# Optimization experiments

Measured on AMD Instinct MI355X. Metric: run time of the kernel, lower is better.

The kernel has to match this reference:

```python
import jax, jax.numpy as jnp
import numpy as np

EMBED_DIM = 768
NUM_HEADS = 12
HEAD_DIM = EMBED_DIM // NUM_HEADS
SCALE = HEAD_DIM ** -0.5


def setup_inputs() -> dict:
    key = jax.random.key(0)
    ks = jax.random.split(key, 9)
    B, S, D = 2, 2048, EMBED_DIM
    init = 1.0 / np.sqrt(D)  # ~ nn.Linear default uniform scale
    x = jax.random.normal(ks[0], (B, S, D), dtype=jnp.float32)
    Wq = jax.random.uniform(ks[1], (D, D), jnp.float32, -init, init)
    bq = jax.random.uniform(ks[2], (D,), jnp.float32, -init, init)
    Wk = jax.random.uniform(ks[3], (D, D), jnp.float32, -init, init)
    bk = jax.random.uniform(ks[4], (D,), jnp.float32, -init, init)
    Wv = jax.random.uniform(ks[5], (D, D), jnp.float32, -init, init)
    bv = jax.random.uniform(ks[6], (D,), jnp.float32, -init, init)
    Wo = jax.random.uniform(ks[7], (D, D), jnp.float32, -init, init)
    bo = jax.random.uniform(ks[8], (D,), jnp.float32, -init, init)
    return {"x": x, "Wq": Wq, "bq": bq, "Wk": Wk, "bk": bk,
            "Wv": Wv, "bv": bv, "Wo": Wo, "bo": bo}


def reference(x, Wq, bq, Wk, bk, Wv, bv, Wo, bo):
    B, S, D = x.shape
    H, Dh = NUM_HEADS, HEAD_DIM
    # projections; weights stored as (in, out) so x @ W == torch Linear with W.T
    q = (x @ Wq + bq).reshape(B, S, H, Dh).transpose(0, 2, 1, 3)  # [B,H,S,Dh]
    k = (x @ Wk + bk).reshape(B, S, H, Dh).transpose(0, 2, 1, 3)
    v = (x @ Wv + bv).reshape(B, S, H, Dh).transpose(0, 2, 1, 3)
    scores = jnp.einsum("bhqd,bhkd->bhqk", q, k) * SCALE        # [B,H,S,S]
    weights = jax.nn.softmax(scores, axis=-1)
    out = jnp.einsum("bhqk,bhkd->bhqd", weights, v)              # [B,H,S,Dh]
    out = out.transpose(0, 2, 1, 3).reshape(B, S, D)
    return out @ Wo + bo
```

## Files before the change

### kernel.cpp

```cpp
#include <hip/hip_runtime.h>
#include <math.h>

#define BB 2
#define SS 2048
#define DDIM 768
#define HH 12
#define DH 64
#define NROWS (BB*SS)
#define NQT2 (SS/128)
#define NSPLIT 4

typedef _Float16 f16;
typedef _Float16 half2v __attribute__((ext_vector_type(2)));
typedef __fp16 fp16x2 __attribute__((ext_vector_type(2)));
typedef _Float16 half4 __attribute__((ext_vector_type(4)));
typedef _Float16 half8 __attribute__((ext_vector_type(8)));
typedef float f32x4 __attribute__((ext_vector_type(4)));
typedef float f32x16 __attribute__((ext_vector_type(16)));
typedef unsigned int u32;
typedef unsigned int u32x4v __attribute__((ext_vector_type(4)));

__device__ __forceinline__ half2v cvt_pk_f16(float a, float b) {
    fp16x2 t = __builtin_amdgcn_cvt_pkrtz(a, b);
    return __builtin_bit_cast(half2v, t);
}

#define MFMA16(a,b,c) __builtin_amdgcn_mfma_f32_16x16x32_f16((a),(b),(c),0,0,0)
#define MFMA32(a,b,c) __builtin_amdgcn_mfma_f32_32x32x16_f16((a),(b),(c),0,0,0)
#define QSCALE (0.125f * 1.44269504088896f)
#define M_STATIC 10.0f

__device__ __forceinline__ int swz(int row, int chunk16) {
    return row*128 + ((chunk16 ^ (row & 7)) << 4);
}

__global__ __launch_bounds__(256) void prep_w(const float* __restrict__ Wq, const float* __restrict__ Wk,
                                              const float* __restrict__ Wv, const float* __restrict__ Wo,
                                              f16* __restrict__ Wt)
{
    const int z = blockIdx.z;
    const float* W = z==0 ? Wq : (z==1 ? Wk : (z==2 ? Wv : Wo));
    f16* out = Wt + (size_t)z * DDIM * DDIM;

    __shared__ float tile[64][65];
    const int t = threadIdx.x;
    const int k0 = blockIdx.x*64, n0 = blockIdx.y*64;

    const int kr = t >> 2, nc = (t & 3) * 16;
    #pragma unroll
    for (int i = 0; i < 4; ++i) {
        float4 v = *(const float4*)&W[(size_t)(k0+kr)*DDIM + n0 + nc + i*4];
        tile[kr][nc+i*4+0] = v.x; tile[kr][nc+i*4+1] = v.y;
        tile[kr][nc+i*4+2] = v.z; tile[kr][nc+i*4+3] = v.w;
    }
    __syncthreads();
    const int nr = t >> 2, kc = (t & 3) * 16;
    half8 h0, h1;
    #pragma unroll
    for (int j = 0; j < 8; ++j) {
        h0[j] = (f16)tile[kc + j][nr];
        h1[j] = (f16)tile[kc + 8 + j][nr];
    }
    *(half8*)&out[(size_t)(n0+nr)*DDIM + k0 + kc]     = h0;
    *(half8*)&out[(size_t)(n0+nr)*DDIM + k0 + kc + 8] = h1;
}

__global__ __launch_bounds__(256) void proj_qkv(const float* __restrict__ x, const f16* __restrict__ Wt,
        const float* __restrict__ bq, const float* __restrict__ bk, const float* __restrict__ bv,
        f16* __restrict__ qb, f16* __restrict__ kb2, f16* __restrict__ vtb)
{
    const int z = blockIdx.z;
    const f16* Wz = Wt + (size_t)z * DDIM * DDIM;
    const float* bias = z==0 ? bq : (z==1 ? bk : bv);
    const float qscale = (z==0) ? QSCALE : 1.0f;

    __shared__ __align__(16) unsigned char lds[24*1024];
    unsigned char* As = lds;
    unsigned char* Bs = lds + 8192;

    const int tid = threadIdx.x;
    const int l = tid & 63, w = tid >> 6;
    const int g = l >> 4, qi = l & 15;
    const int wm = w >> 1, wn = w & 1;
    const int m0 = blockIdx.x * 64, n0 = blockIdx.y * 128;

    f32x4 acc[2][4];
    #pragma unroll
    for (int i=0;i<2;i++)
        #pragma unroll
        for (int j=0;j<4;j++) { f32x4 zv = {0.f,0.f,0.f,0.f}; acc[i][j] = zv; }

    half8 sa[2], sb[4];

#define GLOAD(t) { \
        _Pragma("unroll") \
        for (int i = 0; i < 2; ++i) { \
            int c = i*256 + tid, row = c >> 3, kc = c & 7; \
            const float* xp = &x[(size_t)(m0+row)*DDIM + (t)*64 + kc*8]; \
            float4 a0 = *(const float4*)xp; \
            float4 a1 = *(const float4*)(xp + 4); \
            half8 hv = {(f16)a0.x,(f16)a0.y,(f16)a0.z,(f16)a0.w, \
                        (f16)a1.x,(f16)a1.y,(f16)a1.z,(f16)a1.w}; \
            sa[i] = hv; \
        } \
        _Pragma("unroll") \
        for (int i = 0; i < 4; ++i) { \
            int c = i*256 + tid, row = c >> 3, kc = c & 7; \
            sb[i] = *(const half8*)&Wz[(size_t)(n0+row)*DDIM + (t)*64 + kc*8]; \
        } }

#define GWRT { \
        _Pragma("unroll") \
        for (int i = 0; i < 2; ++i) { \
            int c = i*256 + tid, row = c >> 3, kc = c & 7; \
            *(half8*)(As + swz(row, kc)) = sa[i]; \
        } \
        _Pragma("unroll") \
        for (int i = 0; i < 4; ++i) { \
            int c = i*256 + tid, row = c >> 3, kc = c & 7; \
            *(half8*)(Bs + swz(row, kc)) = sb[i]; \
        } }

    GLOAD(0); GWRT;
    __syncthreads();

    for (int t = 0; t < 12; ++t) {
        if (t < 11) GLOAD(t+1);

        half8 af[2][2], bf[4][2];
        #pragma unroll
        for (int mt = 0; mt < 2; ++mt) {
            int row = wm*32 + mt*16 + qi;
            #pragma unroll
            for (int kh = 0; kh < 2; ++kh)
                af[mt][kh] = *(const half8*)(As + swz(row, kh*4 + g));
        }
        #pragma unroll
        for (int nt = 0; nt < 4; ++nt) {
            int row = wn*64 + nt*16 + qi;
            #pragma unroll
            for (int kh = 0; kh < 2; ++kh)
                bf[nt][kh] = *(const half8*)(Bs + swz(row, kh*4 + g));
        }
        __builtin_amdgcn_s_setprio(1);
        #pragma unroll
        for (int mt = 0; mt < 2; ++mt)
            #pragma unroll
            for (int nt = 0; nt < 4; ++nt) {
                acc[mt][nt] = MFMA16(af[mt][0], bf[nt][0], acc[mt][nt]);
                acc[mt][nt] = MFMA16(af[mt][1], bf[nt][1], acc[mt][nt]);
            }
        __builtin_amdgcn_s_setprio(0);

        if (t < 11) {
            __syncthreads();
            GWRT;
            __syncthreads();
        }
    }

    if (z == 2) {
        #pragma unroll
        for (int mt = 0; mt < 2; ++mt)
            #pragma unroll
            for (int nt = 0; nt < 4; ++nt) {
                int m = m0 + wm*32 + mt*16 + g*4;
                int n = n0 + wn*64 + nt*16 + qi;
                int b = m >> 11, s = m & 2047;
                int h = n >> 6,  d = n & 63;
                float bs = bias[n];
                half4 o4 = {(f16)(acc[mt][nt][0] + bs), (f16)(acc[mt][nt][1] + bs),
                            (f16)(acc[mt][nt][2] + bs), (f16)(acc[mt][nt][3] + bs)};
                *(half4*)&vtb[(((size_t)(b*HH + h))*DH + d)*SS + s] = o4;
            }
    } else {
        f16* out = (z == 0) ? qb : kb2;
        #pragma unroll
        for (int mt = 0; mt < 2; ++mt)
            #pragma unroll
            for (int nt = 0; nt < 4; ++nt)
                #pragma unroll
                for (int r = 0; r < 4; ++r) {
                    int m = m0 + wm*32 + mt*16 + g*4 + r;
                    int n = n0 + wn*64 + nt*16 + qi;
                    float v = (acc[mt][nt][r] + bias[n]) * qscale;
                    int b = m >> 11, s = m & 2047;
                    int h = n >> 6,  d = n & 63;
                    out[(((size_t)(b*HH + h))*SS + s)*DH + d] = (f16)v;
                }
    }
#undef GLOAD
#undef GWRT
}

__global__ __launch_bounds__(256) void attn_mfma(
        const f16* __restrict__ qbuf, const f16* __restrict__ kbuf,
        const f16* __restrict__ vtbuf, f16* __restrict__ pO, float* __restrict__ mlb)
{
    __shared__ __align__(16) unsigned char lds[32*1024];

    const int tid = threadIdx.x;
    const int l = tid & 63, w = tid >> 6;
    const int q31 = l & 31, hl = l >> 5;
    const int qt = blockIdx.x, h = blockIdx.y;
    const int b = blockIdx.z >> 2, kq = blockIdx.z & 3;
    const int q0 = qt * 128 + w * 32;
    const size_t base = ((size_t)(b * HH + h)) * SS * DH;
    const int key0 = kq * (SS/NSPLIT);
    const int pid = (b * HH + h) * NQT2 + qt;

    half8 qf[4];
    #pragma unroll
    for (int s = 0; s < 4; ++s)
        qf[s] = *(const half8*)&qbuf[base + (size_t)(q0 + q31)*DH + s*16 + hl*8];

    f32x16 oacc[2];
    #pragma unroll
    for (int dt = 0; dt < 2; ++dt)
        #pragma unroll
        for (int i = 0; i < 16; ++i) oacc[dt][i] = 0.f;
    float lsum = 0.f;
    f32x16 minit16;
    #pragma unroll
    for (int i = 0; i < 16; ++i) minit16[i] = -M_STATIC;

    half8 sk[2], svv[2];

#define LOADT(t) { \
        _Pragma("unroll") \
        for (int i = 0; i < 2; ++i) { \
            int c = i*256 + tid, row = c >> 3, col = c & 7; \
            sk[i]  = *(const half8*)&kbuf[base + (size_t)(key0 + (t)*64 + row)*DH + col*8]; \
            svv[i] = *(const half8*)&vtbuf[base + (size_t)row*SS + key0 + (t)*64 + col*8]; \
        } }

#define WRT(bufi) { \
        unsigned char* Kw_ = lds + (bufi)*16384; \
        unsigned char* Vw_ = Kw_ + 8192; \
        _Pragma("unroll") \
        for (int i = 0; i < 2; ++i) { \
            int c = i*256 + tid, row = c >> 3, col = c & 7; \
            *(half8*)(Kw_ + swz(row, col)) = sk[i]; \
            *(half8*)(Vw_ + swz(row, col)) = svv[i]; \
        } }

    LOADT(0); WRT(0);
    __syncthreads();

    for (int t = 0; t < 8; ++t) {
        const int cur = t & 1;
        if (t < 7) LOADT(t+1);

        const unsigned char* Kb = lds + cur*16384;
        const unsigned char* Vb = Kb + 8192;

        half8 kA[2][4];
        #pragma unroll
        for (int mt = 0; mt < 2; ++mt)
            #pragma unroll
            for (int s = 0; s < 4; ++s)
                kA[mt][s] = *(const half8*)(Kb + swz(mt*32 + q31, 2*s + hl));
        half8 vA[2][4];
        #pragma unroll
        for (int dt = 0; dt < 2; ++dt)
            #pragma unroll
            for (int ks = 0; ks < 4; ++ks)
                vA[dt][ks] = *(const half8*)(Vb + swz(dt*32 + q31, 2*ks + hl));

        half2v ph[16];
        #pragma unroll
        for (int mt = 0; mt < 2; ++mt) {
            __builtin_amdgcn_s_setprio(1);
            f32x16 sv = minit16;
            #pragma unroll
            for (int s = 0; s < 4; ++s)
                sv = MFMA32(kA[mt][s], qf[s], sv);
            __builtin_amdgcn_s_setprio(0);
            #pragma unroll
            for (int r = 0; r < 16; r += 2)
                ph[mt*8 + (r>>1)] = cvt_pk_f16(exp2f(sv[r]), exp2f(sv[r+1]));
        }

        {
            half2v t01 = (ph[0]+ph[1]) + (ph[2]+ph[3]);
            half2v t23 = (ph[4]+ph[5]) + (ph[6]+ph[7]);
            half2v t45 = (ph[8]+ph[9]) + (ph[10]+ph[11]);
            half2v t67 = (ph[12]+ph[13]) + (ph[14]+ph[15]);
            half2v tt = (t01+t23) + (t45+t67);
            float rs = (float)tt[0] + (float)tt[1];
            rs += __shfl_xor(rs, 32);
            lsum += rs;
        }

        half8 pf[4];
        #pragma unroll
        for (int ks = 0; ks < 4; ++ks) {
            u32 x0 = __builtin_bit_cast(u32, ph[4*ks + 0]);
            u32 x2 = __builtin_bit_cast(u32, ph[4*ks + 2]);
            asm volatile("v_permlane32_swap_b32 %0, %1" : "+v"(x0), "+v"(x2));
            u32 x1 = __builtin_bit_cast(u32, ph[4*ks + 1]);
            u32 x3 = __builtin_bit_cast(u32, ph[4*ks + 3]);
            asm volatile("v_permlane32_swap_b32 %0, %1" : "+v"(x1), "+v"(x3));
            u32x4v tv = {x0, x1, x2, x3};
            pf[ks] = __builtin_bit_cast(half8, tv);
        }

        __builtin_amdgcn_s_setprio(1);
        #pragma unroll
        for (int dt = 0; dt < 2; ++dt)
            #pragma unroll
            for (int ks = 0; ks < 4; ++ks)
                oacc[dt] = MFMA32(vA[dt][ks], pf[ks], oacc[dt]);
        __builtin_amdgcn_s_setprio(0);

        if (t < 7) WRT(cur^1);
        __syncthreads();
    }

    f16* po = pO + ((size_t)pid*NSPLIT + kq) * (128*64);
    float* mlp = mlb + ((size_t)pid*NSPLIT + kq) * 128;
    const int qw = w*32 + q31;
    const float inv = 1.0f / lsum;
    #pragma unroll
    for (int dt = 0; dt < 2; ++dt)
        #pragma unroll
        for (int g2 = 0; g2 < 4; ++g2) {
            half4 o4 = {(f16)(oacc[dt][g2*4+0]*inv), (f16)(oacc[dt][g2*4+1]*inv),
                        (f16)(oacc[dt][g2*4+2]*inv), (f16)(oacc[dt][g2*4+3]*inv)};
            *(half4*)&po[qw*64 + dt*32 + g2*8 + hl*4] = o4;
        }
    if (hl == 0) mlp[qw] = lsum;
#undef LOADT
#undef WRT
}

__global__ __launch_bounds__(256) void attn_combine(
        const f16* __restrict__ pO, const float* __restrict__ mlb, f16* __restrict__ ob)
{
    const int gr = blockIdx.x*64 + (threadIdx.x >> 2);
    const int dg = (threadIdx.x & 3) << 4;
    const int bh = gr >> 11, s = gr & 2047;
    const int qt = s >> 7, qr = s & 127;
    const int pid = bh * NQT2 + qt;

    float lv[NSPLIT], lt = 0.f;
    #pragma unroll
    for (int i = 0; i < NSPLIT; ++i) {
        lv[i] = mlb[((size_t)pid*NSPLIT + i)*128 + qr];
        lt += lv[i];
    }
    const float inv = 1.0f / lt;

    float a0[8] = {}, a1[8] = {};
    #pragma unroll
    for (int i = 0; i < NSPLIT; ++i) {
        const f16* Oi = pO + ((size_t)pid*NSPLIT + i)*(128*64) + qr*64 + dg;
        half8 x0 = *(const half8*)Oi;
        half8 x1 = *(const half8*)(Oi + 8);
        float wi = lv[i] * inv;
        #pragma unroll
        for (int j = 0; j < 8; ++j) {
            a0[j] += wi * (float)x0[j];
            a1[j] += wi * (float)x1[j];
        }
    }
    half8 r0, r1;
    #pragma unroll
    for (int j = 0; j < 8; ++j) { r0[j] = (f16)a0[j]; r1[j] = (f16)a1[j]; }
    f16* dst = &ob[((size_t)bh*SS + s)*DH + dg];
    *(half8*)dst = r0;
    *(half8*)(dst + 8) = r1;
}

__global__ __launch_bounds__(256) void proj_out(const f16* __restrict__ obuf, const f16* __restrict__ Wt,
                                                const float* __restrict__ bo, float* __restrict__ out)
{
    const f16* Wz = Wt + (size_t)3 * DDIM * DDIM;

    __shared__ __align__(16) unsigned char lds[24*1024];
    unsigned char* As = lds;
    unsigned char* Bs = lds + 8192;

    const int tid = threadIdx.x;
    const int l = tid & 63, w = tid >> 6;
    const int g = l >> 4, qi = l & 15;
    const int wm = w >> 1, wn = w & 1;
    const int m0 = blockIdx.x * 64, n0 = blockIdx.y * 128;

    f32x4 acc[2][4];
    #pragma unroll
    for (int i=0;i<2;i++)
        #pragma unroll
        for (int j=0;j<4;j++) { f32x4 zv = {0.f,0.f,0.f,0.f}; acc[i][j] = zv; }

    half8 sa[2], sb[4];

#define GLOAD(t) { \
        _Pragma("unroll") \
        for (int i = 0; i < 2; ++i) { \
            int c = i*256 + tid, row = c >> 3, kc = c & 7; \
            int m = m0 + row, bb_ = m >> 11, ss_ = m & 2047; \
            sa[i] = *(const half8*)&obuf[(((size_t)(bb_*HH + (t)))*SS + ss_)*DH + kc*8]; \
        } \
        _Pragma("unroll") \
        for (int i = 0; i < 4; ++i) { \
            int c = i*256 + tid, row = c >> 3, kc = c & 7; \
            sb[i] = *(const half8*)&Wz[(size_t)(n0+row)*DDIM + (t)*64 + kc*8]; \
        } }

#define GWRT { \
        _Pragma("unroll") \
        for (int i = 0; i < 2; ++i) { \
            int c = i*256 + tid, row = c >> 3, kc = c & 7; \
            *(half8*)(As + swz(row, kc)) = sa[i]; \
        } \
        _Pragma("unroll") \
        for (int i = 0; i < 4; ++i) { \
            int c = i*256 + tid, row = c >> 3, kc = c & 7; \
            *(half8*)(Bs + swz(row, kc)) = sb[i]; \
        } }

    GLOAD(0); GWRT;
    __syncthreads();

    for (int t = 0; t < 12; ++t) {
        if (t < 11) GLOAD(t+1);

        half8 af[2][2], bf[4][2];
        #pragma unroll
        for (int mt = 0; mt < 2; ++mt) {
            int row = wm*32 + mt*16 + qi;
            #pragma unroll
            for (int kh = 0; kh < 2; ++kh)
                af[mt][kh] = *(const half8*)(As + swz(row, kh*4 + g));
        }
        #pragma unroll
        for (int nt = 0; nt < 4; ++nt) {
            int row = wn*64 + nt*16 + qi;
            #pragma unroll
            for (int kh = 0; kh < 2; ++kh)
                bf[nt][kh] = *(const half8*)(Bs + swz(row, kh*4 + g));
        }
        __builtin_amdgcn_s_setprio(1);
        #pragma unroll
        for (int mt = 0; mt < 2; ++mt)
            #pragma unroll
            for (int nt = 0; nt < 4; ++nt) {
                acc[mt][nt] = MFMA16(af[mt][0], bf[nt][0], acc[mt][nt]);
                acc[mt][nt] = MFMA16(af[mt][1], bf[nt][1], acc[mt][nt]);
            }
        __builtin_amdgcn_s_setprio(0);

        if (t < 11) {
            __syncthreads();
            GWRT;
            __syncthreads();
        }
    }

    #pragma unroll
    for (int mt = 0; mt < 2; ++mt)
        #pragma unroll
        for (int nt = 0; nt < 4; ++nt)
            #pragma unroll
            for (int r = 0; r < 4; ++r) {
                int m = m0 + wm*32 + mt*16 + g*4 + r;
                int n = n0 + wn*64 + nt*16 + qi;
                out[(size_t)m*DDIM + n] = acc[mt][nt][r] + bo[n];
            }
#undef GLOAD
#undef GWRT
}

extern "C" void kernel_launch(void* const* d_in, const int* in_sizes, int n_in,
                              void* d_out, int out_size, void* d_ws, size_t ws_size,
                              hipStream_t stream)
{
    const float* x  = (const float*)d_in[0];
    const float* Wq = (const float*)d_in[1];
    const float* bq = (const float*)d_in[2];
    const float* Wk = (const float*)d_in[3];
    const float* bk = (const float*)d_in[4];
    const float* Wv = (const float*)d_in[5];
    const float* bv = (const float*)d_in[6];
    const float* Wo = (const float*)d_in[7];
    const float* bo = (const float*)d_in[8];

    char* ws = (char*)d_ws;
    const size_t WT_B  = (size_t)4 * DDIM * DDIM * 2;
    const size_t HB_B  = (size_t)BB * HH * SS * DH * 2;
    const size_t PO_B  = (size_t)BB * HH * NQT2 * NSPLIT * 128 * 64 * 2;
    const size_t ML_B  = (size_t)BB * HH * NQT2 * NSPLIT * 128 * 4;

    f16* Wt = (f16*)ws;
    f16* qb = (f16*)(ws + WT_B);
    f16* kb = (f16*)(ws + WT_B + HB_B);
    f16* vt = (f16*)(ws + WT_B + 2*HB_B);
    f16* pO = (f16*)(ws + WT_B + 3*HB_B);
    float* mlb = (float*)(ws + WT_B + 3*HB_B + PO_B);
    f16* ob = (f16*)(ws + WT_B + 3*HB_B + PO_B + ML_B);

    prep_w<<<dim3(DDIM/64, DDIM/64, 4), 256, 0, stream>>>(Wq, Wk, Wv, Wo, Wt);
    proj_qkv<<<dim3(NROWS/64, DDIM/128, 3), 256, 0, stream>>>(x, Wt, bq, bk, bv, qb, kb, vt);
    attn_mfma<<<dim3(NQT2, HH, BB*NSPLIT), 256, 0, stream>>>(qb, kb, vt, pO, mlb);
    attn_combine<<<dim3(BB*HH*SS/64), 256, 0, stream>>>(pO, mlb, ob);
    proj_out<<<dim3(NROWS/64, DDIM/128), 256, 0, stream>>>(ob, Wt, bo, (float*)d_out);
}
```

Measured before the change: 116.7 us.

## Use single-wave attention blocks with direct global-to-LDS async loads

The attention kernel goes from 4-wave blocks sharing K/V tiles to one-wave blocks of 32 queries. Each block now loads its own K/V tiles with global_load_lds straight into a single LDS buffer, so the register staging, double buffering and block-wide barriers are gone. The next tile's load is issued once the current tile has been read into registers. In exchange, K/V traffic from global memory and L2 goes up fourfold because tiles are no longer shared across waves, and the load is exposed at the start of each iteration.

```diff
diff --git a/kernel.cpp b/kernel.cpp
--- a/kernel.cpp
+++ b/kernel.cpp
@@ -23,6 +23,12 @@
 __device__ __forceinline__ half2v cvt_pk_f16(float a, float b) {
     fp16x2 t = __builtin_amdgcn_cvt_pkrtz(a, b);
     return __builtin_bit_cast(half2v, t);
+}
+
+__device__ __forceinline__ void gload16(const void* g, void* l) {
+    __builtin_amdgcn_global_load_lds(
+        (const __attribute__((address_space(1))) unsigned int*)(g),
+        (__attribute__((address_space(3))) unsigned int*)(l), 16, 0, 0);
 }
 
 #define MFMA16(a,b,c) __builtin_amdgcn_mfma_f32_16x16x32_f16((a),(b),(c),0,0,0)
@@ -193,21 +199,26 @@
 #undef GWRT
 }
 
-__global__ __launch_bounds__(256) void attn_mfma(
+__global__ __launch_bounds__(64) void attn_mfma(
         const f16* __restrict__ qbuf, const f16* __restrict__ kbuf,
         const f16* __restrict__ vtbuf, f16* __restrict__ pO, float* __restrict__ mlb)
 {
-    __shared__ __align__(16) unsigned char lds[32*1024];
-
-    const int tid = threadIdx.x;
-    const int l = tid & 63, w = tid >> 6;
+    __shared__ __align__(16) unsigned char lds[16*1024];
+    unsigned char* Kl = lds;
+    unsigned char* Vl = lds + 8192;
+
+    const int l = threadIdx.x;
     const int q31 = l & 31, hl = l >> 5;
-    const int qt = blockIdx.x, h = blockIdx.y;
+    const int lrow = l >> 3;
+    const int colc = (l & 7) ^ (lrow & 7);
+    const int qt = blockIdx.x;
+    const int h = blockIdx.y;
     const int b = blockIdx.z >> 2, kq = blockIdx.z & 3;
-    const int q0 = qt * 128 + w * 32;
+    const int q0 = qt * 32;
     const size_t base = ((size_t)(b * HH + h)) * SS * DH;
     const int key0 = kq * (SS/NSPLIT);
-    const int pid = (b * HH + h) * NQT2 + qt;
+    const int pid = (b * HH + h) * NQT2 + (qt >> 2);
+    const int qw = (qt & 3) * 32 + q31;
 
     half8 qf[4];
     #pragma unroll
@@ -224,48 +235,36 @@
     #pragma unroll
     for (int i = 0; i < 16; ++i) minit16[i] = -M_STATIC;
 
-    half8 sk[2], svv[2];
-
-#define LOADT(t) { \
-        _Pragma("unroll") \
-        for (int i = 0; i < 2; ++i) { \
-            int c = i*256 + tid, row = c >> 3, col = c & 7; \
-            sk[i]  = *(const half8*)&kbuf[base + (size_t)(key0 + (t)*64 + row)*DH + col*8]; \
-            svv[i] = *(const half8*)&vtbuf[base + (size_t)row*SS + key0 + (t)*64 + col*8]; \
-        } }
-
-#define WRT(bufi) { \
-        unsigned char* Kw_ = lds + (bufi)*16384; \
-        unsigned char* Vw_ = Kw_ + 8192; \
-        _Pragma("unroll") \
-        for (int i = 0; i < 2; ++i) { \
-            int c = i*256 + tid, row = c >> 3, col = c & 7; \
-            *(half8*)(Kw_ + swz(row, col)) = sk[i]; \
-            *(half8*)(Vw_ + swz(row, col)) = svv[i]; \
-        } }
-
-    LOADT(0); WRT(0);
-    __syncthreads();
+#define GLDS(t) { \
+        _Pragma("unroll") \
+        for (int i = 0; i < 8; ++i) \
+            gload16(&kbuf[base + (size_t)(key0 + (t)*64 + i*8 + lrow)*DH + colc*8], Kl + i*1024); \
+        _Pragma("unroll") \
+        for (int i = 0; i < 8; ++i) \
+            gload16(&vtbuf[base + (size_t)(i*8 + lrow)*SS + key0 + (t)*64 + colc*8], Vl + i*1024); }
+
+    GLDS(0);
 
     for (int t = 0; t < 8; ++t) {
-        const int cur = t & 1;
-        if (t < 7) LOADT(t+1);
-
-        const unsigned char* Kb = lds + cur*16384;
-        const unsigned char* Vb = Kb + 8192;
+        asm volatile("s_waitcnt vmcnt(0)" ::: "memory");
+        __builtin_amdgcn_sched_barrier(0);
 
         half8 kA[2][4];
         #pragma unroll
         for (int mt = 0; mt < 2; ++mt)
             #pragma unroll
             for (int s = 0; s < 4; ++s)
-                kA[mt][s] = *(const half8*)(Kb + swz(mt*32 + q31, 2*s + hl));
+                kA[mt][s] = *(const half8*)(Kl + swz(mt*32 + q31, 2*s + hl));
         half8 vA[2][4];
         #pragma unroll
         for (int dt = 0; dt < 2; ++dt)
             #pragma unroll
             for (int ks = 0; ks < 4; ++ks)
-                vA[dt][ks] = *(const half8*)(Vb + swz(dt*32 + q31, 2*ks + hl));
+                vA[dt][ks] = *(const half8*)(Vl + swz(dt*32 + q31, 2*ks + hl));
+
+        asm volatile("s_waitcnt lgkmcnt(0)" ::: "memory");
+        __builtin_amdgcn_sched_barrier(0);
+        if (t < 7) GLDS(t+1);
 
         half2v ph[16];
         #pragma unroll
@@ -312,14 +311,10 @@
             for (int ks = 0; ks < 4; ++ks)
                 oacc[dt] = MFMA32(vA[dt][ks], pf[ks], oacc[dt]);
         __builtin_amdgcn_s_setprio(0);
-
-        if (t < 7) WRT(cur^1);
-        __syncthreads();
     }
 
     f16* po = pO + ((size_t)pid*NSPLIT + kq) * (128*64);
     float* mlp = mlb + ((size_t)pid*NSPLIT + kq) * 128;
-    const int qw = w*32 + q31;
     const float inv = 1.0f / lsum;
     #pragma unroll
     for (int dt = 0; dt < 2; ++dt)
@@ -330,8 +325,7 @@
             *(half4*)&po[qw*64 + dt*32 + g2*8 + hl*4] = o4;
         }
     if (hl == 0) mlp[qw] = lsum;
-#undef LOADT
-#undef WRT
+#undef GLDS
 }
 
 __global__ __launch_bounds__(256) void attn_combine(
@@ -502,7 +496,7 @@
 
     prep_w<<<dim3(DDIM/64, DDIM/64, 4), 256, 0, stream>>>(Wq, Wk, Wv, Wo, Wt);
     proj_qkv<<<dim3(NROWS/64, DDIM/128, 3), 256, 0, stream>>>(x, Wt, bq, bk, bv, qb, kb, vt);
-    attn_mfma<<<dim3(NQT2, HH, BB*NSPLIT), 256, 0, stream>>>(qb, kb, vt, pO, mlb);
+    attn_mfma<<<dim3(SS/32, HH, BB*NSPLIT), 64, 0, stream>>>(qb, kb, vt, pO, mlb);
     attn_combine<<<dim3(BB*HH*SS/64), 256, 0, stream>>>(pO, mlb, ob);
     proj_out<<<dim3(NROWS/64, DDIM/128), 256, 0, stream>>>(ob, Wt, bo, (float*)d_out);
 }
```

New measurement: 121.2 us. 1.04x slower.

## Stream K/V tiles directly to LDS with triple-buffered async global_load_lds

Applied to the files above, without the earlier changes.

Replaces the register-staged K/V load-then-LDS-write double buffer in the attention kernel with direct global-to-LDS loads (global_load_lds, 16 bytes per lane) into a three-stage ring buffer, prefetching two tiles ahead. The swizzle is reproduced through the per-lane source column so the LDS layout stays the same. Synchronization becomes one vmcnt wait plus a barrier per tile instead of a write and a syncthreads. This removes VGPR staging and LDS store instructions and deepens prefetch, at the cost of 48KB of LDS per block, which may lower occupancy.

```diff
diff --git a/kernel.cpp b/kernel.cpp
--- a/kernel.cpp
+++ b/kernel.cpp
@@ -23,6 +23,12 @@
 __device__ __forceinline__ half2v cvt_pk_f16(float a, float b) {
     fp16x2 t = __builtin_amdgcn_cvt_pkrtz(a, b);
     return __builtin_bit_cast(half2v, t);
+}
+
+__device__ __forceinline__ void gload16(const void* g, void* l) {
+    __builtin_amdgcn_global_load_lds(
+        (const __attribute__((address_space(1))) unsigned int*)(g),
+        (__attribute__((address_space(3))) unsigned int*)(l), 16, 0, 0);
 }
 
 #define MFMA16(a,b,c) __builtin_amdgcn_mfma_f32_16x16x32_f16((a),(b),(c),0,0,0)
@@ -197,11 +203,12 @@
         const f16* __restrict__ qbuf, const f16* __restrict__ kbuf,
         const f16* __restrict__ vtbuf, f16* __restrict__ pO, float* __restrict__ mlb)
 {
-    __shared__ __align__(16) unsigned char lds[32*1024];
+    __shared__ __align__(16) unsigned char lds[48*1024];
 
     const int tid = threadIdx.x;
     const int l = tid & 63, w = tid >> 6;
     const int q31 = l & 31, hl = l >> 5;
+    const int colc = (l & 7) ^ (l >> 3);
     const int qt = blockIdx.x, h = blockIdx.y;
     const int b = blockIdx.z >> 2, kq = blockIdx.z & 3;
     const int q0 = qt * 128 + w * 32;
@@ -213,6 +220,8 @@
     #pragma unroll
     for (int s = 0; s < 4; ++s)
         qf[s] = *(const half8*)&qbuf[base + (size_t)(q0 + q31)*DH + s*16 + hl*8];
+    asm volatile("s_waitcnt vmcnt(0)" ::: "memory");
+    __builtin_amdgcn_sched_barrier(0);
 
     f32x16 oacc[2];
     #pragma unroll
@@ -224,34 +233,27 @@
     #pragma unroll
     for (int i = 0; i < 16; ++i) minit16[i] = -M_STATIC;
 
-    half8 sk[2], svv[2];
-
-#define LOADT(t) { \
+#define GLDS(t, bo_) { \
+        unsigned char* Kd_ = lds + (bo_); \
+        unsigned char* Vd_ = Kd_ + 8192; \
         _Pragma("unroll") \
         for (int i = 0; i < 2; ++i) { \
-            int c = i*256 + tid, row = c >> 3, col = c & 7; \
-            sk[i]  = *(const half8*)&kbuf[base + (size_t)(key0 + (t)*64 + row)*DH + col*8]; \
-            svv[i] = *(const half8*)&vtbuf[base + (size_t)row*SS + key0 + (t)*64 + col*8]; \
+            int row = (w*2 + i)*8 + (l >> 3); \
+            gload16(&kbuf[base + (size_t)(key0 + (t)*64 + row)*DH + colc*8], Kd_ + (w*2+i)*1024); \
+            gload16(&vtbuf[base + (size_t)row*SS + key0 + (t)*64 + colc*8], Vd_ + (w*2+i)*1024); \
         } }
 
-#define WRT(bufi) { \
-        unsigned char* Kw_ = lds + (bufi)*16384; \
-        unsigned char* Vw_ = Kw_ + 8192; \
-        _Pragma("unroll") \
-        for (int i = 0; i < 2; ++i) { \
-            int c = i*256 + tid, row = c >> 3, col = c & 7; \
-            *(half8*)(Kw_ + swz(row, col)) = sk[i]; \
-            *(half8*)(Vw_ + swz(row, col)) = svv[i]; \
-        } }
-
-    LOADT(0); WRT(0);
-    __syncthreads();
+    GLDS(0, 0);
+    GLDS(1, 16384);
 
     for (int t = 0; t < 8; ++t) {
-        const int cur = t & 1;
-        if (t < 7) LOADT(t+1);
-
-        const unsigned char* Kb = lds + cur*16384;
+        const int bo = (t % 3) * 16384;
+        if (t < 7) asm volatile("s_waitcnt vmcnt(4)" ::: "memory");
+        else       asm volatile("s_waitcnt vmcnt(0)" ::: "memory");
+        __builtin_amdgcn_s_barrier();
+        __builtin_amdgcn_sched_barrier(0);
+
+        const unsigned char* Kb = lds + bo;
         const unsigned char* Vb = Kb + 8192;
 
         half8 kA[2][4];
@@ -266,6 +268,10 @@
             #pragma unroll
             for (int ks = 0; ks < 4; ++ks)
                 vA[dt][ks] = *(const half8*)(Vb + swz(dt*32 + q31, 2*ks + hl));
+
+        asm volatile("s_waitcnt lgkmcnt(0)" ::: "memory");
+        __builtin_amdgcn_sched_barrier(0);
+        if (t < 6) GLDS(t+2, ((t+2) % 3) * 16384);
 
         half2v ph[16];
         #pragma unroll
@@ -312,9 +318,6 @@
             for (int ks = 0; ks < 4; ++ks)
                 oacc[dt] = MFMA32(vA[dt][ks], pf[ks], oacc[dt]);
         __builtin_amdgcn_s_setprio(0);
-
-        if (t < 7) WRT(cur^1);
-        __syncthreads();
     }
 
     f16* po = pO + ((size_t)pid*NSPLIT + kq) * (128*64);
@@ -330,8 +333,7 @@
             *(half4*)&po[qw*64 + dt*32 + g2*8 + hl*4] = o4;
         }
     if (hl == 0) mlp[qw] = lsum;
-#undef LOADT
-#undef WRT
+#undef GLDS
 }
 
 __global__ __launch_bounds__(256) void attn_combine(
```

Result: no change. 116.0 us (-0.6%).
